# Kernel tuning notes

Hardware: AMD Instinct MI355X
Metric: run time of the kernel (lower is better)

The kernel has to match this reference:

```python
import jax, jax.numpy as jnp
import numpy as np


def setup_inputs() -> dict:
    key = jax.random.key(0)
    ks = jax.random.split(key, 5)
    D, H, S, B = 2048, 16, 2048, 2
    kd = D // H
    scale = 0.02
    return {
        "in_x": jax.random.normal(ks[0], (B, S, D), dtype=jnp.float32),
        "W_sc": jax.random.normal(ks[1], (D, D), dtype=jnp.float32) * scale,
        "b_sc": jax.random.normal(ks[2], (D,), dtype=jnp.float32) * scale,
        "W_qkv": jax.random.normal(ks[3], (D, D + 2 * kd), dtype=jnp.float32) * scale,
        "b_qkv": jax.random.normal(ks[4], (D + 2 * kd,), dtype=jnp.float32) * scale,
        "head_num": 16,
    }


def reference(in_x, W_sc, b_sc, W_qkv, b_qkv, head_num):
    B, S, D = in_x.shape
    kd = D // head_num
    # two independent linear projections
    short_cut = in_x @ W_sc + b_sc                      # [B,S,D]
    qkv = in_x @ W_qkv + b_qkv                          # [B,S,D+2*kd]
    q = qkv[..., :D].reshape(B, S, head_num, kd).transpose(0, 2, 1, 3)  # [B,H,S,kd]
    k = qkv[..., D:D + kd]                              # [B,S,kd] shared single K head
    v = qkv[..., D + kd:]                               # [B,S,kd] shared single V head
    # NOTE: faithful to source, scale is k_dim**2, not sqrt(k_dim)
    score = jnp.einsum("bhsd,btd->bhst", q, k) / float(kd * kd)         # [B,H,S,S]
    atten = jnp.einsum("bhst,btd->bhsd", jax.nn.softmax(score, axis=-1), v)  # [B,H,S,kd]
    res = atten.transpose(0, 2, 1, 3).reshape(B, S, D)  # [B,S,D]
    return (score, atten, res, short_cut)
```

## Files before the change

kernel.cpp:

```cpp
#include <hip/hip_runtime.h>
#include <math.h>

#define M_    4096
#define D_    2048
#define NQKV  2304
#define KD_   128
#define S_    2048

using bf16x8  = __attribute__((ext_vector_type(8))) __bf16;
using f32x4   = __attribute__((ext_vector_type(4))) float;
using ushort8 = __attribute__((ext_vector_type(8))) unsigned short;

__device__ __forceinline__ unsigned short f2bf(float f) {
  unsigned int u = __builtin_bit_cast(unsigned int, f);
  u += 0x7fffu + ((u >> 16) & 1u);
  return (unsigned short)(u >> 16);
}
__device__ __forceinline__ unsigned int pack2bf(float a, float b) {
  return (unsigned int)f2bf(a) | ((unsigned int)f2bf(b) << 16);
}

#define GLL16(g, l) \
  __builtin_amdgcn_global_load_lds((__attribute__((address_space(1))) void*)(g), \
                                   (__attribute__((address_space(3))) void*)(l), 16, 0, 0)

__global__ void cast_x_kernel(const float* __restrict__ x, unsigned short* __restrict__ xb) {
  int i = (blockIdx.x * 256 + threadIdx.x) * 8;
  float4 a = *(const float4*)(x + i);
  float4 b = *(const float4*)(x + i + 4);
  ushort8 o;
  o[0]=f2bf(a.x); o[1]=f2bf(a.y); o[2]=f2bf(a.z); o[3]=f2bf(a.w);
  o[4]=f2bf(b.x); o[5]=f2bf(b.y); o[6]=f2bf(b.z); o[7]=f2bf(b.w);
  *(ushort8*)(xb + i) = o;
}

__global__ void prep_w_kernel(const float* __restrict__ Wsc, const float* __restrict__ Wqkv,
                              unsigned short* __restrict__ Wt) {
  __shared__ float t[32][33];
  int k0 = blockIdx.x * 32, n0 = blockIdx.y * 32;
  int tx = threadIdx.x, ty = threadIdx.y;
  #pragma unroll
  for (int i = 0; i < 32; i += 8) {
    int k = k0 + ty + i, n = n0 + tx;
    t[ty + i][tx] = (n < D_) ? Wsc[(size_t)k * D_ + n] : Wqkv[(size_t)k * NQKV + (n - D_)];
  }
  __syncthreads();
  #pragma unroll
  for (int i = 0; i < 32; i += 8) {
    int n = n0 + ty + i, k = k0 + tx;
    Wt[(size_t)n * D_ + k] = f2bf(t[tx][ty + i]);
  }
}

__global__ __launch_bounds__(256, 2) void gemm_fused_kernel(
    const unsigned short* __restrict__ X,
    const unsigned short* __restrict__ Wt,
    const float* __restrict__ b_sc, const float* __restrict__ b_qkv,
    float* __restrict__ shortcut, unsigned short* __restrict__ qkv) {
  __shared__ alignas(16) unsigned short As[128 * 32];
  __shared__ alignas(16) unsigned short Bs[128 * 32];
  const int tid = threadIdx.x;
  const int lane = tid & 63, wid = tid >> 6;
  const int l16 = lane & 15, quad = lane >> 4;
  const int wm = (wid >> 1) * 64, wn = (wid & 1) * 64;
  const int bid = blockIdx.x;
  const int wg = (bid & 7) * 136 + (bid >> 3);
  const int m0 = (wg / 34) * 128, n0 = (wg % 34) * 128;

  const int fa = tid * 16;
  const char* aSrc0 = (const char*)X  + (size_t)(m0 + (fa >> 6)) * 4096 + (fa & 63);
  const char* aSrc1 = aSrc0 + (size_t)64 * 4096;
  const char* bSrc0 = (const char*)Wt + (size_t)(n0 + (fa >> 6)) * 4096 + (fa & 63);
  const char* bSrc1 = bSrc0 + (size_t)64 * 4096;
  char* aDst0 = (char*)As + fa; char* aDst1 = aDst0 + 4096;
  char* bDst0 = (char*)Bs + fa; char* bDst1 = bDst0 + 4096;

  f32x4 acc[4][4] = {};
  for (int kt = 0; kt < 64; ++kt) {
    __syncthreads();
    GLL16(aSrc0, aDst0); GLL16(aSrc1, aDst1);
    GLL16(bSrc0, bDst0); GLL16(bSrc1, bDst1);
    aSrc0 += 64; aSrc1 += 64; bSrc0 += 64; bSrc1 += 64;
    __syncthreads();
    bf16x8 af[4], bfr[4];
    #pragma unroll
    for (int mi = 0; mi < 4; ++mi)
      af[mi] = *(const bf16x8*)(As + (wm + mi * 16 + l16) * 32 + quad * 8);
    #pragma unroll
    for (int ni = 0; ni < 4; ++ni)
      bfr[ni] = *(const bf16x8*)(Bs + (wn + ni * 16 + l16) * 32 + quad * 8);
    #pragma unroll
    for (int mi = 0; mi < 4; ++mi)
      #pragma unroll
      for (int ni = 0; ni < 4; ++ni)
        acc[mi][ni] = __builtin_amdgcn_mfma_f32_16x16x32_bf16(af[mi], bfr[ni], acc[mi][ni], 0, 0, 0);
  }

  #pragma unroll
  for (int ni = 0; ni < 4; ++ni) {
    int n = n0 + wn + ni * 16 + l16;
    float bias = (n < D_) ? b_sc[n] : b_qkv[n - D_];
    #pragma unroll
    for (int mi = 0; mi < 4; ++mi) {
      #pragma unroll
      for (int r = 0; r < 4; ++r) {
        int m = m0 + wm + mi * 16 + quad * 4 + r;
        float v = acc[mi][ni][r] + bias;
        if (n < D_) shortcut[(size_t)m * D_ + n] = v;
        else        qkv[(size_t)m * NQKV + (n - D_)] = f2bf(v);
      }
    }
  }
}

__global__ void prep_vt_kernel(const unsigned short* __restrict__ qkv,
                               unsigned short* __restrict__ vt) {
  __shared__ unsigned short t[32][33];
  int b = blockIdx.z;
  int t0 = blockIdx.x * 32, d0 = blockIdx.y * 32;
  int tx = threadIdx.x, ty = threadIdx.y;
  #pragma unroll
  for (int i = 0; i < 32; i += 8)
    t[ty + i][tx] = qkv[(size_t)(b * S_ + t0 + ty + i) * NQKV + (D_ + KD_) + d0 + tx];
  __syncthreads();
  #pragma unroll
  for (int i = 0; i < 32; i += 8)
    vt[(size_t)(b * KD_ + d0 + ty + i) * S_ + t0 + tx] = t[tx][ty + i];
}

__global__ __launch_bounds__(256, 2) void attn_kernel(
    const unsigned short* __restrict__ qkv,
    const unsigned short* __restrict__ vt,
    float* __restrict__ score, float* __restrict__ atten, float* __restrict__ res) {
  __shared__ alignas(16) unsigned short Ks[4 * 128 * 32];
  __shared__ alignas(16) unsigned short Vs[4 * 128 * 32];
  __shared__ alignas(16) unsigned short Ps[4 * 64 * 32];

  const int tid = threadIdx.x;
  const int lane = tid & 63, wid = tid >> 6;
  const int l16 = lane & 15, quad = lane >> 4;
  const int bid = blockIdx.x;
  const int wg = (bid & 7) * 128 + (bid >> 3);
  const int qt = wg & 31, bh = wg >> 5;
  const int b = bh >> 4, h = bh & 15;
  const int q0 = qt * 64;
  const int rr = tid >> 2, cc = (tid & 3) * 16;

  bf16x8 qf[4];
  {
    const unsigned short* qb = qkv + (size_t)(b * S_ + q0 + wid * 16 + l16) * NQKV + h * KD_ + quad * 8;
    #pragma unroll
    for (int kk = 0; kk < 4; ++kk) qf[kk] = *(const bf16x8*)(qb + kk * 32);
  }

  f32x4 acc_o[8] = {};
  float m_r = -1e30f, l_r = 0.f;
  const float inv_scale = 1.0f / 16384.0f;

  const char* kb0 = (const char*)qkv + (size_t)b * S_ * (NQKV * 2) + D_ * 2;
  const char* vb0 = (const char*)vt + (size_t)b * KD_ * S_ * 2;

  for (int tt = 0; tt < 16; ++tt) {
    const int t0 = tt * 128;
    __syncthreads();
    #pragma unroll
    for (int i = 0; i < 8; ++i) {
      int kk = i >> 1, t = (i & 1) * 64 + rr;
      GLL16(kb0 + (size_t)(t0 + t) * (NQKV * 2) + kk * 64 + cc, (char*)Ks + i * 4096 + tid * 16);
    }
    #pragma unroll
    for (int i = 0; i < 8; ++i) {
      int kkt = i >> 1, d = (i & 1) * 64 + rr;
      GLL16(vb0 + (size_t)d * (S_ * 2) + t0 * 2 + kkt * 64 + cc, (char*)Vs + i * 4096 + tid * 16);
    }
    __syncthreads();

    f32x4 sa[8], sb[8];
    #pragma unroll
    for (int jt = 0; jt < 8; ++jt) {
      f32x4 a = {};
      #pragma unroll
      for (int kk = 0; kk < 4; ++kk) {
        bf16x8 kf = *(const bf16x8*)(Ks + kk * 4096 + (jt * 16 + l16) * 32 + quad * 8);
        a = __builtin_amdgcn_mfma_f32_16x16x32_bf16(kf, qf[kk], a, 0, 0, 0);
      }
      #pragma unroll
      for (int r = 0; r < 4; ++r) a[r] *= inv_scale;
      sa[jt] = a; sb[jt] = a;
    }

    float mx = sa[0][0];
    #pragma unroll
    for (int jt = 0; jt < 8; ++jt)
      #pragma unroll
      for (int r = 0; r < 4; ++r) mx = fmaxf(mx, sa[jt][r]);
    mx = fmaxf(mx, __shfl_xor(mx, 16));
    mx = fmaxf(mx, __shfl_xor(mx, 32));
    float mn = fmaxf(m_r, mx);
    float alpha = __expf(m_r - mn);
    m_r = mn;
    float sm = 0.f;
    #pragma unroll
    for (int jt = 0; jt < 8; ++jt)
      #pragma unroll
      for (int r = 0; r < 4; ++r) { float p = __expf(sa[jt][r] - mn); sa[jt][r] = p; sm += p; }
    sm += __shfl_xor(sm, 16);
    sm += __shfl_xor(sm, 32);
    l_r = l_r * alpha + sm;
    float al[4];
    #pragma unroll
    for (int r = 0; r < 4; ++r) al[r] = __shfl(alpha, quad * 4 + r);
    #pragma unroll
    for (int dn = 0; dn < 8; ++dn)
      #pragma unroll
      for (int r = 0; r < 4; ++r) acc_o[dn][r] *= al[r];

    {
      const int qrow = wid * 16 + l16;
      #pragma unroll
      for (int jt = 0; jt < 8; ++jt) {
        uint2 w; w.x = pack2bf(sa[jt][0], sa[jt][1]); w.y = pack2bf(sa[jt][2], sa[jt][3]);
        *(uint2*)(Ps + (jt >> 1) * 2048 + qrow * 32 + (jt & 1) * 16 + quad * 4) = w;
      }
    }

    {
      float* sc = score + ((size_t)bh * S_ + q0 + wid * 16 + l16) * S_ + t0 + quad * 4;
      #pragma unroll
      for (int jt = 0; jt < 8; ++jt) *(f32x4*)(sc + jt * 16) = sb[jt];
    }

    #pragma unroll
    for (int kkt = 0; kkt < 4; ++kkt) {
      bf16x8 pf = *(const bf16x8*)(Ps + kkt * 2048 + (wid * 16 + l16) * 32 + quad * 8);
      #pragma unroll
      for (int dn = 0; dn < 8; ++dn) {
        bf16x8 vf = *(const bf16x8*)(Vs + kkt * 4096 + (dn * 16 + l16) * 32 + quad * 8);
        acc_o[dn] = __builtin_amdgcn_mfma_f32_16x16x32_bf16(pf, vf, acc_o[dn], 0, 0, 0);
      }
    }
  }

  float lo[4];
  #pragma unroll
  for (int r = 0; r < 4; ++r) lo[r] = 1.0f / __shfl(l_r, quad * 4 + r);
  #pragma unroll
  for (int dn = 0; dn < 8; ++dn) {
    int d = dn * 16 + l16;
    #pragma unroll
    for (int r = 0; r < 4; ++r) {
      int q = q0 + wid * 16 + quad * 4 + r;
      float v = acc_o[dn][r] * lo[r];
      atten[((size_t)bh * S_ + q) * KD_ + d] = v;
      res[((size_t)b * S_ + q) * D_ + h * KD_ + d] = v;
    }
  }
}

extern "C" void kernel_launch(void* const* d_in, const int* in_sizes, int n_in,
                              void* d_out, int out_size, void* d_ws, size_t ws_size,
                              hipStream_t stream) {
  (void)in_sizes; (void)n_in; (void)out_size; (void)ws_size;
  const float* in_x  = (const float*)d_in[0];
  const float* W_sc  = (const float*)d_in[1];
  const float* b_sc  = (const float*)d_in[2];
  const float* W_qkv = (const float*)d_in[3];
  const float* b_qkv = (const float*)d_in[4];

  char* ws = (char*)d_ws;
  unsigned short* Xb  = (unsigned short*)ws;
  unsigned short* Wt  = (unsigned short*)(ws + 16777216);
  unsigned short* qkv = (unsigned short*)(ws + 16777216 + 17825792);
  unsigned short* Vt  = (unsigned short*)(ws + 16777216 + 17825792 + 18874368);

  float* score    = (float*)d_out;
  float* atten    = score + 134217728;
  float* res      = atten + 8388608;
  float* shortcut = res + 8388608;

  cast_x_kernel<<<4096, 256, 0, stream>>>(in_x, Xb);
  prep_w_kernel<<<dim3(64, 136), dim3(32, 8), 0, stream>>>(W_sc, W_qkv, Wt);
  gemm_fused_kernel<<<1088, 256, 0, stream>>>(Xb, Wt, b_sc, b_qkv, shortcut, qkv);
  prep_vt_kernel<<<dim3(64, 4, 2), dim3(32, 8), 0, stream>>>(qkv, Vt);
  attn_kernel<<<1024, 256, 0, stream>>>(qkv, Vt, score, atten, res);
}
```

Baseline: 908.9 us.

## Double-buffer K/V tiles and stage score writes through swizzled LDS

The attention loop now uses 64-key tiles with double-buffered K/V staging: the next tile's async global-to-LDS loads are issued before computing on the current tile, which removes one barrier per iteration. Score tiles are transposed through a swizzled LDS scratch (reusing the P buffer) so each row is written to global memory as contiguous float4 runs with nontemporal stores, replacing the strided per-lane writes. The change adds LDS reuse hazards that depend on compiler fences rather than barriers, and it doubles the number of loop iterations and softmax rescale steps.

```diff
diff --git a/kernel.cpp b/kernel.cpp
--- a/kernel.cpp
+++ b/kernel.cpp
@@ -23,6 +23,8 @@
 #define GLL16(g, l) \
   __builtin_amdgcn_global_load_lds((__attribute__((address_space(1))) void*)(g), \
                                    (__attribute__((address_space(3))) void*)(l), 16, 0, 0)
+
+#define CFENCE() asm volatile("" ::: "memory")
 
 __global__ void cast_x_kernel(const float* __restrict__ x, unsigned short* __restrict__ xb) {
   int i = (blockIdx.x * 256 + threadIdx.x) * 8;
@@ -132,9 +134,9 @@
     const unsigned short* __restrict__ qkv,
     const unsigned short* __restrict__ vt,
     float* __restrict__ score, float* __restrict__ atten, float* __restrict__ res) {
-  __shared__ alignas(16) unsigned short Ks[4 * 128 * 32];
-  __shared__ alignas(16) unsigned short Vs[4 * 128 * 32];
-  __shared__ alignas(16) unsigned short Ps[4 * 64 * 32];
+  __shared__ alignas(16) unsigned short Ks[2][4 * 64 * 32];
+  __shared__ alignas(16) unsigned short Vs[2][2 * 128 * 32];
+  __shared__ alignas(16) unsigned short Ps[2 * 64 * 32];
 
   const int tid = threadIdx.x;
   const int lane = tid & 63, wid = tid >> 6;
@@ -159,39 +161,49 @@
 
   const char* kb0 = (const char*)qkv + (size_t)b * S_ * (NQKV * 2) + D_ * 2;
   const char* vb0 = (const char*)vt + (size_t)b * KD_ * S_ * 2;
-
-  for (int tt = 0; tt < 16; ++tt) {
-    const int t0 = tt * 128;
-    __syncthreads();
-    #pragma unroll
-    for (int i = 0; i < 8; ++i) {
-      int kk = i >> 1, t = (i & 1) * 64 + rr;
-      GLL16(kb0 + (size_t)(t0 + t) * (NQKV * 2) + kk * 64 + cc, (char*)Ks + i * 4096 + tid * 16);
-    }
-    #pragma unroll
-    for (int i = 0; i < 8; ++i) {
-      int kkt = i >> 1, d = (i & 1) * 64 + rr;
-      GLL16(vb0 + (size_t)d * (S_ * 2) + t0 * 2 + kkt * 64 + cc, (char*)Vs + i * 4096 + tid * 16);
-    }
-    __syncthreads();
-
-    f32x4 sa[8], sb[8];
-    #pragma unroll
-    for (int jt = 0; jt < 8; ++jt) {
+  float* scr = (float*)Ps;
+
+  #define STAGE_KV(bufi, tbase) do {                                           \
+    char* kd_ = (char*)Ks + (bufi) * 16384 + tid * 16;                         \
+    char* vd_ = (char*)Vs + (bufi) * 16384 + tid * 16;                         \
+    _Pragma("unroll")                                                          \
+    for (int i_ = 0; i_ < 4; ++i_)                                             \
+      GLL16(kb0 + (size_t)((tbase) + rr) * (NQKV * 2) + i_ * 64 + cc,          \
+            kd_ + i_ * 4096);                                                  \
+    _Pragma("unroll")                                                          \
+    for (int i_ = 0; i_ < 4; ++i_)                                             \
+      GLL16(vb0 + (size_t)((i_ & 1) * 64 + rr) * (S_ * 2) + (tbase) * 2        \
+                + (i_ >> 1) * 64 + cc,                                         \
+            vd_ + i_ * 4096);                                                  \
+  } while (0)
+
+  STAGE_KV(0, 0);
+  __syncthreads();
+
+  for (int tt = 0; tt < 32; ++tt) {
+    const int buf = tt & 1;
+    const int t0 = tt * 64;
+    if (tt + 1 < 32) STAGE_KV(buf ^ 1, t0 + 64);
+
+    const unsigned short* ksb = &Ks[buf][0];
+    const unsigned short* vsb = &Vs[buf][0];
+    f32x4 sa[4];
+    #pragma unroll
+    for (int jt = 0; jt < 4; ++jt) {
       f32x4 a = {};
       #pragma unroll
       for (int kk = 0; kk < 4; ++kk) {
-        bf16x8 kf = *(const bf16x8*)(Ks + kk * 4096 + (jt * 16 + l16) * 32 + quad * 8);
+        bf16x8 kf = *(const bf16x8*)(ksb + kk * 2048 + (jt * 16 + l16) * 32 + quad * 8);
         a = __builtin_amdgcn_mfma_f32_16x16x32_bf16(kf, qf[kk], a, 0, 0, 0);
       }
       #pragma unroll
       for (int r = 0; r < 4; ++r) a[r] *= inv_scale;
-      sa[jt] = a; sb[jt] = a;
+      sa[jt] = a;
     }
 
     float mx = sa[0][0];
     #pragma unroll
-    for (int jt = 0; jt < 8; ++jt)
+    for (int jt = 0; jt < 4; ++jt)
       #pragma unroll
       for (int r = 0; r < 4; ++r) mx = fmaxf(mx, sa[jt][r]);
     mx = fmaxf(mx, __shfl_xor(mx, 16));
@@ -199,9 +211,31 @@
     float mn = fmaxf(m_r, mx);
     float alpha = __expf(m_r - mn);
     m_r = mn;
+
+    #pragma unroll
+    for (int hh = 0; hh < 2; ++hh) {
+      #pragma unroll
+      for (int jl = 0; jl < 2; ++jl) {
+        int tp = jl * 16 + quad * 4;
+        int g = l16 * 32 + (tp ^ ((l16 & 7) << 2));
+        *(f32x4*)(scr + (g >> 8) * 1024 + wid * 256 + (g & 255)) = sa[hh * 2 + jl];
+      }
+      CFENCE();
+      #pragma unroll
+      for (int i = 0; i < 2; ++i) {
+        int row = i * 8 + (lane >> 3);
+        int tp = (lane & 7) * 4;
+        int g = row * 32 + (tp ^ ((row & 7) << 2));
+        f32x4 vv = *(const f32x4*)(scr + (g >> 8) * 1024 + wid * 256 + (g & 255));
+        float* dst = score + ((size_t)bh * S_ + q0 + wid * 16 + row) * S_ + t0 + hh * 32 + tp;
+        __builtin_nontemporal_store(vv, (f32x4*)dst);
+      }
+      CFENCE();
+    }
+
     float sm = 0.f;
     #pragma unroll
-    for (int jt = 0; jt < 8; ++jt)
+    for (int jt = 0; jt < 4; ++jt)
       #pragma unroll
       for (int r = 0; r < 4; ++r) { float p = __expf(sa[jt][r] - mn); sa[jt][r] = p; sm += p; }
     sm += __shfl_xor(sm, 16);
@@ -218,28 +252,26 @@
     {
       const int qrow = wid * 16 + l16;
       #pragma unroll
-      for (int jt = 0; jt < 8; ++jt) {
+      for (int jt = 0; jt < 4; ++jt) {
         uint2 w; w.x = pack2bf(sa[jt][0], sa[jt][1]); w.y = pack2bf(sa[jt][2], sa[jt][3]);
         *(uint2*)(Ps + (jt >> 1) * 2048 + qrow * 32 + (jt & 1) * 16 + quad * 4) = w;
       }
     }
-
-    {
-      float* sc = score + ((size_t)bh * S_ + q0 + wid * 16 + l16) * S_ + t0 + quad * 4;
-      #pragma unroll
-      for (int jt = 0; jt < 8; ++jt) *(f32x4*)(sc + jt * 16) = sb[jt];
-    }
-
-    #pragma unroll
-    for (int kkt = 0; kkt < 4; ++kkt) {
+    CFENCE();
+
+    #pragma unroll
+    for (int kkt = 0; kkt < 2; ++kkt) {
       bf16x8 pf = *(const bf16x8*)(Ps + kkt * 2048 + (wid * 16 + l16) * 32 + quad * 8);
       #pragma unroll
       for (int dn = 0; dn < 8; ++dn) {
-        bf16x8 vf = *(const bf16x8*)(Vs + kkt * 4096 + (dn * 16 + l16) * 32 + quad * 8);
+        bf16x8 vf = *(const bf16x8*)(vsb + kkt * 4096 + (dn * 16 + l16) * 32 + quad * 8);
         acc_o[dn] = __builtin_amdgcn_mfma_f32_16x16x32_bf16(pf, vf, acc_o[dn], 0, 0, 0);
       }
     }
-  }
+
+    __syncthreads();
+  }
+  #undef STAGE_KV
 
   float lo[4];
   #pragma unroll
```

New measurement: 861.9 us. 1.05x faster.
